# Kernel optimization log

Measured on AMD Instinct MI355X. Metric: run time of the kernel, lower is better.

Reference implementation:

```python
import jax, jax.numpy as jnp
import numpy as np

V, D, L, FF = 32000, 1024, 6, 4096
B, T = 2, 1024
EPS = 1e-6


def bitlinear(x, W):
    # W: [out, in]. Ternary quantize with straight-through estimator.
    s = jnp.maximum(jnp.mean(jnp.abs(W), axis=1, keepdims=True), 1e-5)
    w_q = jnp.clip(jnp.round(W / s), -1.0, 1.0)
    w = W + jax.lax.stop_gradient(w_q * s - W)
    return x @ w.T


def rmsnorm(x, g):
    return x * jax.lax.rsqrt(jnp.mean(x * x, axis=-1, keepdims=True) + EPS) * g


def time_mix(x, Wr, Wk, Wv, Wo, decay, lnx_w):
    # x: [B,T,D]
    r = jax.nn.sigmoid(bitlinear(x, Wr))
    k = bitlinear(x, Wk)
    v = bitlinear(x, Wv)
    dec = jax.nn.sigmoid(decay)                          # [D]
    log_decay = jnp.log(jnp.maximum(dec, 1e-7))          # [D]
    pos = jnp.arange(x.shape[1], dtype=x.dtype)          # [T]
    scale = jnp.exp(pos[:, None] * log_decay[None, :])   # [T,D]
    scaled = (k * v) / jnp.maximum(scale, 1e-10)[None]   # [B,T,D]
    state = jnp.cumsum(scaled, axis=1) * scale[None]     # [B,T,D]
    return bitlinear(rmsnorm(r * state, lnx_w), Wo)


def channel_mix(x, W1, W2, Wo):
    return bitlinear(jax.nn.silu(bitlinear(x, W1)) * bitlinear(x, W2), Wo)


def setup_inputs() -> dict:
    key = jax.random.key(0)
    ks = jax.random.split(key, 8)
    idx = jax.random.randint(ks[0], (B, T), 0, V)
    embed = jax.random.normal(ks[1], (V, D), jnp.float32) * 0.02

    def kaiming(k, shape):  # fan_out init: std = sqrt(2/out_features)
        return jax.random.normal(k, shape, jnp.float32) * np.sqrt(2.0 / shape[-2])

    kr, kk, kv, ko, k1, k2, koc = jax.random.split(ks[2], 7)
    return {
        "idx": idx,
        "embed": embed,
        "ln_in_w": jnp.ones((D,), jnp.float32),
        "ln1_w": jnp.ones((L, D), jnp.float32),
        "Wr": kaiming(kr, (L, D, D)),
        "Wk": kaiming(kk, (L, D, D)),
        "Wv": kaiming(kv, (L, D, D)),
        "Wo_t": kaiming(ko, (L, D, D)),
        "decay": jnp.full((L, D), 0.99, jnp.float32),
        "lnx_w": jnp.ones((L, D), jnp.float32),
        "ln2_w": jnp.ones((L, D), jnp.float32),
        "W1": kaiming(k1, (L, FF, D)),
        "W2": kaiming(k2, (L, FF, D)),
        "Wo_c": kaiming(koc, (L, D, FF)),
        "ln_out_w": jnp.ones((D,), jnp.float32),
    }


def reference(idx, embed, ln_in_w, ln1_w, Wr, Wk, Wv, Wo_t, decay, lnx_w,
              ln2_w, W1, W2, Wo_c, ln_out_w):
    h = rmsnorm(embed[idx], ln_in_w)  # [B,T,D]
    for i in range(L):
        h = h + time_mix(rmsnorm(h, ln1_w[i]), Wr[i], Wk[i], Wv[i], Wo_t[i],
                         decay[i], lnx_w[i])
        h = h + channel_mix(rmsnorm(h, ln2_w[i]), W1[i], W2[i], Wo_c[i])
    # weight-tied head
    return rmsnorm(h, ln_out_w) @ embed.T  # [B,T,V]
```

## Files before the change

kernel.cpp:

```cpp
#include <hip/hip_runtime.h>

typedef _Float16 f16;
typedef _Float16 f16x8 __attribute__((ext_vector_type(8)));
typedef _Float16 f16x4 __attribute__((ext_vector_type(4)));
typedef float f32x4 __attribute__((ext_vector_type(4)));
typedef int i32x4 __attribute__((ext_vector_type(4)));

static constexpr int BB = 2, T = 1024, D = 1024, FFD = 4096, V = 32000, NL = 6;
static constexpr int M = BB * T;
static constexpr int ROWS_PER_LAYER = 4*D + 2*FFD + D;
static constexpr size_t QL = 4ull*D*D + 2ull*FFD*D + (size_t)D*FFD;
static constexpr int NT = 64, CT = T / NT;
static constexpr int RKV = 3*D;

__device__ __forceinline__ void gload16(const f16* g, f16* l) {
  __builtin_amdgcn_global_load_lds(
      (const __attribute__((address_space(1))) void*)g,
      (__attribute__((address_space(3))) void*)l, 16, 0, 0);
}
__device__ __forceinline__ void gload16b(const void* g, void* l) {
  __builtin_amdgcn_global_load_lds(
      (const __attribute__((address_space(1))) void*)g,
      (__attribute__((address_space(3))) void*)l, 16, 0, 0);
}
template<int N> __device__ __forceinline__ void vm_wait() {
  static_assert(N >= 2 && N <= 4, "unsupported vmcnt");
  if constexpr (N == 2) asm volatile("s_waitcnt vmcnt(2)" ::: "memory");
  else if constexpr (N == 3) asm volatile("s_waitcnt vmcnt(3)" ::: "memory");
  else                       asm volatile("s_waitcnt vmcnt(4)" ::: "memory");
}
__device__ __forceinline__ void ring_barrier() {
  __builtin_amdgcn_s_barrier();
  __builtin_amdgcn_sched_barrier(0);
}

__global__ __launch_bounds__(256) void quant_kernel(
    const float* __restrict__ Wr, const float* __restrict__ Wk,
    const float* __restrict__ Wv, const float* __restrict__ Wo,
    const float* __restrict__ W1, const float* __restrict__ W2,
    const float* __restrict__ Woc, char* __restrict__ qw, float* __restrict__ scales)
{
  const int r = blockIdx.x, l = blockIdx.y;
  const float* base; int len; size_t dst;
  if (r < 4*D) {
    const int m = r >> 10, row = r & (D-1);
    const float* Wm = (m==0) ? Wr : (m==1) ? Wk : (m==2) ? Wv : Wo;
    base = Wm + (size_t)l*D*D + (size_t)row*D; len = D;
    dst = (size_t)l*QL + (size_t)m*D*D + (size_t)row*D;
  } else if (r < 4*D + 2*FFD) {
    int row = r - 4*D;
    const int m = row >= FFD; if (m) row -= FFD;
    const float* Wm = m ? W2 : W1;
    base = Wm + (size_t)l*FFD*D + (size_t)row*D; len = D;
    dst = (size_t)l*QL + 4ull*D*D + (size_t)m*FFD*D + (size_t)row*D;
  } else {
    const int row = r - (4*D + 2*FFD);
    base = Woc + (size_t)l*D*FFD + (size_t)row*FFD; len = FFD;
    dst = (size_t)l*QL + 4ull*D*D + 2ull*FFD*D + (size_t)row*FFD;
  }
  const int nv = len >> 10;
  float4 rv[4];
  float sum = 0.f;
  #pragma unroll 4
  for (int i = 0; i < 4; ++i) {
    if (i < nv) {
      rv[i] = reinterpret_cast<const float4*>(base)[threadIdx.x + i*256];
      sum += fabsf(rv[i].x) + fabsf(rv[i].y) + fabsf(rv[i].z) + fabsf(rv[i].w);
    }
  }
  #pragma unroll
  for (int off = 32; off > 0; off >>= 1) sum += __shfl_down(sum, off);
  __shared__ float red[4]; __shared__ float sbc;
  if ((threadIdx.x & 63) == 0) red[threadIdx.x >> 6] = sum;
  __syncthreads();
  if (threadIdx.x == 0) {
    const float s = fmaxf((red[0]+red[1]+red[2]+red[3]) / (float)len, 1e-5f);
    sbc = s;
    scales[(size_t)l*ROWS_PER_LAYER + r] = s;
  }
  __syncthreads();
  const float hs = 0.5f * sbc;
  #pragma unroll 4
  for (int i = 0; i < 4; ++i) {
    if (i < nv) {
      const float4 v = rv[i];
      char4 q;
      q.x = v.x > hs ? 1 : (v.x < -hs ? -1 : 0);
      q.y = v.y > hs ? 1 : (v.y < -hs ? -1 : 0);
      q.z = v.z > hs ? 1 : (v.z < -hs ? -1 : 0);
      q.w = v.w > hs ? 1 : (v.w < -hs ? -1 : 0);
      reinterpret_cast<char4*>(qw + dst)[threadIdx.x + i*256] = q;
    }
  }
}

__global__ __launch_bounds__(256) void quant_embed_kernel(
    const float* __restrict__ embed, char* __restrict__ q, float* __restrict__ sw)
{
  const int row = blockIdx.x;
  const float4 v = reinterpret_cast<const float4*>(embed + (size_t)row*D)[threadIdx.x];
  float mx = fmaxf(fmaxf(fabsf(v.x), fabsf(v.y)), fmaxf(fabsf(v.z), fabsf(v.w)));
  #pragma unroll
  for (int off = 32; off > 0; off >>= 1) mx = fmaxf(mx, __shfl_down(mx, off));
  __shared__ float red[4]; __shared__ float sbc;
  if ((threadIdx.x & 63) == 0) red[threadIdx.x >> 6] = mx;
  __syncthreads();
  if (threadIdx.x == 0) {
    const float m = fmaxf(fmaxf(red[0], red[1]), fmaxf(red[2], red[3]));
    const float s = fmaxf(m, 1e-8f) * (1.f/127.f);
    sbc = 1.f / s;
    sw[row] = s;
  }
  __syncthreads();
  const float inv = sbc;
  char4 o;
  o.x = (char)__float2int_rn(v.x * inv); o.y = (char)__float2int_rn(v.y * inv);
  o.z = (char)__float2int_rn(v.z * inv); o.w = (char)__float2int_rn(v.w * inv);
  reinterpret_cast<char4*>(q + (size_t)row*D)[threadIdx.x] = o;
}

__global__ __launch_bounds__(256) void embed_rms_kernel(
    const int* __restrict__ idx, const float* __restrict__ embed,
    const float* __restrict__ g, float* __restrict__ h)
{
  const int row = blockIdx.x;
  const int tok = idx[row];
  const float4 xv = reinterpret_cast<const float4*>(embed + (size_t)tok*D)[threadIdx.x];
  float ss = xv.x*xv.x + xv.y*xv.y + xv.z*xv.z + xv.w*xv.w;
  #pragma unroll
  for (int off = 32; off > 0; off >>= 1) ss += __shfl_down(ss, off);
  __shared__ float red[4];
  if ((threadIdx.x & 63) == 0) red[threadIdx.x >> 6] = ss;
  __syncthreads();
  const float mean = (red[0]+red[1]+red[2]+red[3]) * (1.f/(float)D);
  const float rn = rsqrtf(mean + 1e-6f);
  const float4 gv = reinterpret_cast<const float4*>(g)[threadIdx.x];
  float4 ov;
  ov.x = xv.x*rn*gv.x; ov.y = xv.y*rn*gv.y; ov.z = xv.z*rn*gv.z; ov.w = xv.w*rn*gv.w;
  reinterpret_cast<float4*>(h + (size_t)row*D)[threadIdx.x] = ov;
}

__global__ __launch_bounds__(256) void rms_i8_kernel(
    const float* __restrict__ x, const float* __restrict__ g,
    char* __restrict__ q, float* __restrict__ sx)
{
  const int row = blockIdx.x;
  const float4 xv = reinterpret_cast<const float4*>(x + (size_t)row*D)[threadIdx.x];
  const float4 gv = reinterpret_cast<const float4*>(g)[threadIdx.x];
  float4 pv;
  pv.x = xv.x*gv.x; pv.y = xv.y*gv.y; pv.z = xv.z*gv.z; pv.w = xv.w*gv.w;
  float ss = xv.x*xv.x + xv.y*xv.y + xv.z*xv.z + xv.w*xv.w;
  float mg = fmaxf(fmaxf(fabsf(pv.x), fabsf(pv.y)), fmaxf(fabsf(pv.z), fabsf(pv.w)));
  #pragma unroll
  for (int off = 32; off > 0; off >>= 1) {
    ss += __shfl_down(ss, off);
    mg = fmaxf(mg, __shfl_down(mg, off));
  }
  __shared__ float reds[4], redm[4]; __shared__ float sbc;
  if ((threadIdx.x & 63) == 0) { reds[threadIdx.x >> 6] = ss; redm[threadIdx.x >> 6] = mg; }
  __syncthreads();
  if (threadIdx.x == 0) {
    const float mean = (reds[0]+reds[1]+reds[2]+reds[3]) * (1.f/(float)D);
    const float rn = rsqrtf(mean + 1e-6f);
    const float vmax = rn * fmaxf(fmaxf(redm[0], redm[1]), fmaxf(redm[2], redm[3]));
    const float s = fmaxf(vmax, 1e-8f) * (1.f/127.f);
    sx[row] = s;
    sbc = rn / s;
  }
  __syncthreads();
  const float f = sbc;
  char4 o;
  o.x = (char)__float2int_rn(pv.x * f); o.y = (char)__float2int_rn(pv.y * f);
  o.z = (char)__float2int_rn(pv.z * f); o.w = (char)__float2int_rn(pv.w * f);
  reinterpret_cast<char4*>(q + (size_t)row*D)[threadIdx.x] = o;
}

__global__ __launch_bounds__(256) void rms_radd_i8_kernel(
    float* __restrict__ h, const float* __restrict__ p0,
    const float* __restrict__ p1, const float* __restrict__ g,
    char* __restrict__ q, float* __restrict__ sx)
{
  const int row = blockIdx.x;
  const size_t off = (size_t)row*D/4 + threadIdx.x;
  float4 hv = reinterpret_cast<const float4*>(h)[off];
  const float4 a = reinterpret_cast<const float4*>(p0)[off];
  const float4 b = reinterpret_cast<const float4*>(p1)[off];
  hv.x += a.x + b.x; hv.y += a.y + b.y; hv.z += a.z + b.z; hv.w += a.w + b.w;
  reinterpret_cast<float4*>(h)[off] = hv;
  const float4 gv = reinterpret_cast<const float4*>(g)[threadIdx.x];
  float4 pv;
  pv.x = hv.x*gv.x; pv.y = hv.y*gv.y; pv.z = hv.z*gv.z; pv.w = hv.w*gv.w;
  float ss = hv.x*hv.x + hv.y*hv.y + hv.z*hv.z + hv.w*hv.w;
  float mg = fmaxf(fmaxf(fabsf(pv.x), fabsf(pv.y)), fmaxf(fabsf(pv.z), fabsf(pv.w)));
  #pragma unroll
  for (int o2 = 32; o2 > 0; o2 >>= 1) {
    ss += __shfl_down(ss, o2);
    mg = fmaxf(mg, __shfl_down(mg, o2));
  }
  __shared__ float reds[4], redm[4]; __shared__ float sbc;
  if ((threadIdx.x & 63) == 0) { reds[threadIdx.x >> 6] = ss; redm[threadIdx.x >> 6] = mg; }
  __syncthreads();
  if (threadIdx.x == 0) {
    const float mean = (reds[0]+reds[1]+reds[2]+reds[3]) * (1.f/(float)D);
    const float rn = rsqrtf(mean + 1e-6f);
    const float vmax = rn * fmaxf(fmaxf(redm[0], redm[1]), fmaxf(redm[2], redm[3]));
    const float s = fmaxf(vmax, 1e-8f) * (1.f/127.f);
    sx[row] = s;
    sbc = rn / s;
  }
  __syncthreads();
  const float f = sbc;
  char4 o;
  o.x = (char)__float2int_rn(pv.x * f); o.y = (char)__float2int_rn(pv.y * f);
  o.z = (char)__float2int_rn(pv.z * f); o.w = (char)__float2int_rn(pv.w * f);
  reinterpret_cast<char4*>(q + (size_t)row*D)[threadIdx.x] = o;
}

__global__ __launch_bounds__(256) void quant_ffn_kernel(
    const f16* __restrict__ a, char* __restrict__ q, float* __restrict__ s)
{
  const int row = blockIdx.x;
  const size_t base = (size_t)row*(FFD/4);
  f16x4 v[4];
  float mx = 0.f;
  #pragma unroll
  for (int i = 0; i < 4; ++i) {
    v[i] = reinterpret_cast<const f16x4*>(a)[base + threadIdx.x + i*256];
    #pragma unroll
    for (int j = 0; j < 4; ++j) mx = fmaxf(mx, fabsf((float)v[i][j]));
  }
  #pragma unroll
  for (int off = 32; off > 0; off >>= 1) mx = fmaxf(mx, __shfl_down(mx, off));
  __shared__ float red[4]; __shared__ float sbc;
  if ((threadIdx.x & 63) == 0) red[threadIdx.x >> 6] = mx;
  __syncthreads();
  if (threadIdx.x == 0) {
    const float m = fmaxf(fmaxf(red[0], red[1]), fmaxf(red[2], red[3]));
    const float sr = fmaxf(m, 1e-8f) * (1.f/127.f);
    s[row] = sr;
    sbc = 1.f / sr;
  }
  __syncthreads();
  const float inv = sbc;
  #pragma unroll
  for (int i = 0; i < 4; ++i) {
    char4 o;
    o.x = (char)__float2int_rn((float)v[i][0] * inv);
    o.y = (char)__float2int_rn((float)v[i][1] * inv);
    o.z = (char)__float2int_rn((float)v[i][2] * inv);
    o.w = (char)__float2int_rn((float)v[i][3] * inv);
    reinterpret_cast<char4*>(q)[base + threadIdx.x + i*256] = o;
  }
}

__global__ __launch_bounds__(256) void scan1_kernel(
    const float* __restrict__ k, const float* __restrict__ v, int ld,
    const float* __restrict__ decay, float* __restrict__ part)
{
  const int d = blockIdx.x*256 + threadIdx.x;
  const int c = blockIdx.y, b = blockIdx.z;
  const float dec = 1.f / (1.f + expf(-decay[d]));
  const float ldc = logf(fmaxf(dec, 1e-7f));
  float sum = 0.f;
  const int row0 = b*T + c*CT;
  #pragma unroll 4
  for (int t = 0; t < CT; ++t) {
    const size_t i = (size_t)(row0 + t)*ld + d;
    const float scale = expf((float)(c*CT + t) * ldc);
    sum += (k[i] * v[i]) / fmaxf(scale, 1e-10f);
  }
  part[((size_t)b*NT + c)*D + d] = sum;
}

__global__ __launch_bounds__(256) void scan23_kernel(
    const float* __restrict__ r, const float* __restrict__ k,
    const float* __restrict__ v, int ld, const float* __restrict__ decay,
    const float* __restrict__ part, float* __restrict__ rs)
{
  const int d = blockIdx.x*256 + threadIdx.x;
  const int c = blockIdx.y, b = blockIdx.z;
  const float dec = 1.f / (1.f + expf(-decay[d]));
  const float ldc = logf(fmaxf(dec, 1e-7f));
  float cum = 0.f;
  for (int j = 0; j < c; ++j) cum += part[((size_t)b*NT + j)*D + d];
  const int row0 = b*T + c*CT;
  #pragma unroll 4
  for (int t = 0; t < CT; ++t) {
    const size_t i = (size_t)(row0 + t)*ld + d;
    const float scale = expf((float)(c*CT + t) * ldc);
    cum += (k[i] * v[i]) / fmaxf(scale, 1e-10f);
    rs[(size_t)(row0 + t)*D + d] = r[i] * (cum * scale);
  }
}

__global__ __launch_bounds__(256) void rms_f16_kernel(
    const float* __restrict__ x, const float* __restrict__ g, f16* __restrict__ o)
{
  const int row = blockIdx.x;
  const float4 xv = reinterpret_cast<const float4*>(x + (size_t)row*D)[threadIdx.x];
  float ss = xv.x*xv.x + xv.y*xv.y + xv.z*xv.z + xv.w*xv.w;
  #pragma unroll
  for (int off = 32; off > 0; off >>= 1) ss += __shfl_down(ss, off);
  __shared__ float red[4];
  if ((threadIdx.x & 63) == 0) red[threadIdx.x >> 6] = ss;
  __syncthreads();
  const float mean = (red[0]+red[1]+red[2]+red[3]) * (1.f/(float)D);
  const float rn = rsqrtf(mean + 1e-6f);
  const float4 gv = reinterpret_cast<const float4*>(g)[threadIdx.x];
  f16x4 ov;
  ov[0] = (f16)(xv.x*rn*gv.x); ov[1] = (f16)(xv.y*rn*gv.y);
  ov[2] = (f16)(xv.z*rn*gv.z); ov[3] = (f16)(xv.w*rn*gv.w);
  reinterpret_cast<f16x4*>(o + (size_t)row*D)[threadIdx.x] = ov;
}

__global__ __launch_bounds__(256) void scan2_kernel(float* __restrict__ part)
{
  const int d = blockIdx.x*256 + threadIdx.x;
  const int b = blockIdx.y;
  float run = 0.f;
  #pragma unroll 8
  for (int c = 0; c < NT; ++c) {
    const size_t i = ((size_t)b*NT + c)*D + d;
    const float t = part[i];
    part[i] = run;
    run += t;
  }
}

__global__ __launch_bounds__(256) void scan3_kernel(
    const float* __restrict__ r, const float* __restrict__ k,
    const float* __restrict__ v, int ld, const float* __restrict__ decay,
    const float* __restrict__ part, float* __restrict__ rs)
{
  const int d = blockIdx.x*256 + threadIdx.x;
  const int c = blockIdx.y, b = blockIdx.z;
  const float dec = 1.f / (1.f + expf(-decay[d]));
  const float ldc = logf(fmaxf(dec, 1e-7f));
  float cum = part[((size_t)b*NT + c)*D + d];
  const int row0 = b*T + c*CT;
  #pragma unroll 4
  for (int t = 0; t < CT; ++t) {
    const size_t i = (size_t)(row0 + t)*ld + d;
    const float scale = expf((float)(c*CT + t) * ldc);
    cum += (k[i] * v[i]) / fmaxf(scale, 1e-10f);
    rs[(size_t)(row0 + t)*D + d] = r[i] * (cum * scale);
  }
}

__global__ __launch_bounds__(256) void silumul_kernel(
    const f16* __restrict__ a, const f16* __restrict__ b, f16* __restrict__ o, int n4)
{
  const int i = blockIdx.x*256 + threadIdx.x;
  if (i >= n4) return;
  const f16x4 av = reinterpret_cast<const f16x4*>(a)[i];
  const f16x4 bv = reinterpret_cast<const f16x4*>(b)[i];
  f16x4 ov;
  #pragma unroll
  for (int j = 0; j < 4; ++j) {
    const float x = (float)av[j];
    ov[j] = (f16)((x / (1.f + expf(-x))) * (float)bv[j]);
  }
  reinterpret_cast<f16x4*>(o)[i] = ov;
}

__device__ __forceinline__ int xcd_swizzle(int fid, int nwg) {
  const int q = nwg >> 3, r = nwg & 7, x = fid & 7, o = fid >> 3;
  return (x < r ? x*(q+1) : r*(q+1) + (x-r)*q) + o;
}

template<int BM, int NW, int EPI, bool SPLITK = false>
__global__ __launch_bounds__(NW*64) void gemm_i8_kernel(
    const char* __restrict__ A, const char* __restrict__ Bq,
    const float* __restrict__ sx, const float* __restrict__ scl,
    const float* __restrict__ resid, float* __restrict__ outp, int N, int K)
{
  constexpr int WN = 2;
  constexpr int WM = NW / WN;
  constexpr int MF = BM / (WM*16);
  constexpr int ACALLS = BM / (16*NW);
  constexpr int BCALLS = 128 / (16*NW);
  constexpr int VCNT = ACALLS + BCALLS;
  __shared__ __align__(16) char As[3][BM*64];
  __shared__ __align__(16) char Bs[3][128*64];

  const int tid = threadIdx.x;
  const int wave = tid >> 6, lane = tid & 63;
  const int gx = gridDim.x, nwg = gx * gridDim.y;
  const int wg = xcd_swizzle(blockIdx.x + blockIdx.y*gx, nwg);
  const int m0 = (wg % gx) * BM, n0 = (wg / gx) * 128;
  const int lr = lane & 15, kg = lane >> 4;
  const int wm0 = (wave / WN) * (MF*16), wn0 = (wave % WN) * 64;
  const int grow = lane >> 2;
  const int gcol = (lane & 3) * 16;
  const char* Ab = A  + (size_t)(m0 + grow)*K + gcol;
  const char* Bb = Bq + (size_t)(n0 + grow)*K + gcol;

  int kbeg = 0, kend = K;
  size_t obase = 0;
  if (SPLITK) {
    const int kc = K / gridDim.z;
    kbeg = blockIdx.z * kc; kend = kbeg + kc;
    obase = (size_t)blockIdx.z * M * (size_t)N;
  }
  const int NKT = (kend - kbeg) / 64;

  auto stage = [&](int buf, int k0) {
    #pragma unroll
    for (int c = 0; c < ACALLS; ++c) {
      const int rb = (c*NW + wave) * 16;
      gload16b(Ab + (size_t)rb*K + k0, &As[buf][rb*64]);
    }
    #pragma unroll
    for (int c = 0; c < BCALLS; ++c) {
      const int rb = (c*NW + wave) * 16;
      gload16b(Bb + (size_t)rb*K + k0, &Bs[buf][rb*64]);
    }
  };

  i32x4 acc[MF][4] = {};
  stage(0, kbeg);
  stage(1, kbeg + 64);

  int cur = 0;
  for (int t = 0; t < NKT; ++t) {
    vm_wait<VCNT>();
    ring_barrier();
    if (t + 2 < NKT) {
      int nb = cur + 2; if (nb >= 3) nb -= 3;
      stage(nb, kbeg + (t + 2) * 64);
    }
    i32x4 af[MF], bf[4];
    #pragma unroll
    for (int i = 0; i < MF; ++i)
      af[i] = *reinterpret_cast<const i32x4*>(&As[cur][(wm0 + i*16 + lr)*64 + kg*16]);
    #pragma unroll
    for (int j = 0; j < 4; ++j)
      bf[j] = *reinterpret_cast<const i32x4*>(&Bs[cur][(wn0 + j*16 + lr)*64 + kg*16]);
    #pragma unroll
    for (int i = 0; i < MF; ++i)
      #pragma unroll
      for (int j = 0; j < 4; ++j)
        acc[i][j] = __builtin_amdgcn_mfma_i32_16x16x64_i8(af[i], bf[j], acc[i][j], 0, 0, 0);
    ++cur; if (cur == 3) cur = 0;
  }

  #pragma unroll
  for (int j = 0; j < 4; ++j) {
    const int col = n0 + wn0 + j*16 + lr;
    const float sv = scl[col];
    #pragma unroll
    for (int i = 0; i < MF; ++i) {
      #pragma unroll
      for (int e = 0; e < 4; ++e) {
        const int row = m0 + wm0 + i*16 + kg*4 + e;
        float y = (float)acc[i][j][e] * sx[row] * sv;
        if (EPI == 3 && col < D) y = 1.f / (1.f + expf(-y));
        if (EPI == 2) y += resid[(size_t)row*N + col];
        outp[obase + (size_t)row*N + col] = y;
      }
    }
  }
}

__global__ __launch_bounds__(512) void gemm_head_i8_kernel(
    const char* __restrict__ A, const char* __restrict__ Bq,
    const float* __restrict__ sx, const float* __restrict__ sw,
    float* __restrict__ out, int N, int K)
{
  constexpr int BM = 128, BN = 256;
  __shared__ __align__(16) char As[3][BM*64];
  __shared__ __align__(16) char Bs[3][BN*64];
  const int tid = threadIdx.x;
  const int wave = tid >> 6, lane = tid & 63;
  const int gx = gridDim.x, nwg = gx * gridDim.y;
  const int wg = xcd_swizzle(blockIdx.x + blockIdx.y*gx, nwg);
  const int m0 = (wg % gx) * BM, n0 = (wg / gx) * BN;
  const int lr = lane & 15, kg = lane >> 4;
  const int wm0 = (wave >> 2) * 64, wn0 = (wave & 3) * 64;
  const int grow = lane >> 2;
  const int gcol = (lane & 3) * 16;
  const char* Ab = A  + (size_t)(m0 + grow)*K + gcol;
  const char* Bb = Bq + (size_t)(n0 + grow)*K + gcol;

  auto stage = [&](int buf, int k0) {
    gload16b(Ab + (size_t)(wave*16)*K + k0, &As[buf][(wave*16)*64]);
    gload16b(Bb + (size_t)(wave*16)*K + k0, &Bs[buf][(wave*16)*64]);
    gload16b(Bb + (size_t)((wave+8)*16)*K + k0, &Bs[buf][((wave+8)*16)*64]);
  };

  i32x4 acc[4][4] = {};
  stage(0, 0);
  stage(1, 64);

  const int NKT = K / 64;
  int cur = 0;
  for (int t = 0; t < NKT; ++t) {
    vm_wait<3>();
    ring_barrier();
    if (t + 2 < NKT) {
      int nb = cur + 2; if (nb >= 3) nb -= 3;
      stage(nb, (t + 2) * 64);
    }
    i32x4 af[4], bf[4];
    #pragma unroll
    for (int i = 0; i < 4; ++i)
      af[i] = *reinterpret_cast<const i32x4*>(&As[cur][(wm0 + i*16 + lr)*64 + kg*16]);
    #pragma unroll
    for (int j = 0; j < 4; ++j)
      bf[j] = *reinterpret_cast<const i32x4*>(&Bs[cur][(wn0 + j*16 + lr)*64 + kg*16]);
    #pragma unroll
    for (int i = 0; i < 4; ++i)
      #pragma unroll
      for (int j = 0; j < 4; ++j)
        acc[i][j] = __builtin_amdgcn_mfma_i32_16x16x64_i8(af[i], bf[j], acc[i][j], 0, 0, 0);
    ++cur; if (cur == 3) cur = 0;
  }
  #pragma unroll
  for (int j = 0; j < 4; ++j) {
    const int col = n0 + wn0 + j*16 + lr;
    const float scw = sw[col];
    #pragma unroll
    for (int i = 0; i < 4; ++i) {
      #pragma unroll
      for (int e = 0; e < 4; ++e) {
        const int row = m0 + wm0 + i*16 + kg*4 + e;
        out[(size_t)row*N + col] = (float)acc[i][j][e] * sx[row] * scw;
      }
    }
  }
}

__global__ __launch_bounds__(512) void gemm_ffn_i8_kernel(
    const char* __restrict__ A, const char* __restrict__ B1, const char* __restrict__ B2,
    const float* __restrict__ sx, const float* __restrict__ s1, const float* __restrict__ s2,
    f16* __restrict__ outg, int N, int K)
{
  constexpr int BM = 128, BN = 128;
  __shared__ __align__(16) char As [3][BM*64];
  __shared__ __align__(16) char B1s[3][BN*64];
  __shared__ __align__(16) char B2s[3][BN*64];
  const int tid = threadIdx.x;
  const int wave = tid >> 6, lane = tid & 63;
  const int gx = gridDim.x, nwg = gx * gridDim.y;
  const int wg = xcd_swizzle(blockIdx.x + blockIdx.y*gx, nwg);
  const int m0 = (wg % gx) * BM, n0 = (wg / gx) * BN;
  const int lr = lane & 15, kg = lane >> 4;
  const int wm0 = (wave >> 1) * 32, wn0 = (wave & 1) * 64;
  const int grow = lane >> 2;
  const int gcol = (lane & 3) * 16;
  const char* Ab  = A  + (size_t)(m0 + grow)*K + gcol;
  const char* B1b = B1 + (size_t)(n0 + grow)*K + gcol;
  const char* B2b = B2 + (size_t)(n0 + grow)*K + gcol;

  auto stage = [&](int buf, int k0) {
    const int rb = wave * 16;
    gload16b(Ab  + (size_t)rb*K + k0, &As [buf][rb*64]);
    gload16b(B1b + (size_t)rb*K + k0, &B1s[buf][rb*64]);
    gload16b(B2b + (size_t)rb*K + k0, &B2s[buf][rb*64]);
  };

  i32x4 aca[2][4] = {};
  i32x4 acb[2][4] = {};
  stage(0, 0);
  stage(1, 64);

  const int NKT = K / 64;
  int cur = 0;
  for (int t = 0; t < NKT; ++t) {
    vm_wait<3>();
    ring_barrier();
    if (t + 2 < NKT) {
      int nb = cur + 2; if (nb >= 3) nb -= 3;
      stage(nb, (t + 2) * 64);
    }
    i32x4 af[2], b1f[4], b2f[4];
    #pragma unroll
    for (int i = 0; i < 2; ++i)
      af[i] = *reinterpret_cast<const i32x4*>(&As[cur][(wm0 + i*16 + lr)*64 + kg*16]);
    #pragma unroll
    for (int j = 0; j < 4; ++j) {
      b1f[j] = *reinterpret_cast<const i32x4*>(&B1s[cur][(wn0 + j*16 + lr)*64 + kg*16]);
      b2f[j] = *reinterpret_cast<const i32x4*>(&B2s[cur][(wn0 + j*16 + lr)*64 + kg*16]);
    }
    #pragma unroll
    for (int i = 0; i < 2; ++i)
      #pragma unroll
      for (int j = 0; j < 4; ++j) {
        aca[i][j] = __builtin_amdgcn_mfma_i32_16x16x64_i8(af[i], b1f[j], aca[i][j], 0, 0, 0);
        acb[i][j] = __builtin_amdgcn_mfma_i32_16x16x64_i8(af[i], b2f[j], acb[i][j], 0, 0, 0);
      }
    ++cur; if (cur == 3) cur = 0;
  }
  #pragma unroll
  for (int j = 0; j < 4; ++j) {
    const int col = n0 + wn0 + j*16 + lr;
    const float sa = s1[col], sb = s2[col];
    #pragma unroll
    for (int i = 0; i < 2; ++i) {
      #pragma unroll
      for (int e = 0; e < 4; ++e) {
        const int row = m0 + wm0 + i*16 + kg*4 + e;
        const float srow = sx[row];
        const float a = (float)aca[i][j][e] * srow * sa;
        const float b = (float)acb[i][j][e] * srow * sb;
        outg[(size_t)row*N + col] = (f16)((a / (1.f + expf(-a))) * b);
      }
    }
  }
}

__global__ __launch_bounds__(64) void scales_kernel(
    const float* __restrict__ Wr, const float* __restrict__ Wk,
    const float* __restrict__ Wv, const float* __restrict__ Wo,
    const float* __restrict__ W1, const float* __restrict__ W2,
    const float* __restrict__ Woc, float* __restrict__ s)
{
  const int r = blockIdx.x, l = blockIdx.y;
  const float* base; int len;
  if (r < 4*D) {
    const int m = r >> 10, row = r & (D-1);
    const float* Wm = (m==0) ? Wr : (m==1) ? Wk : (m==2) ? Wv : Wo;
    base = Wm + (size_t)l*D*D + (size_t)row*D; len = D;
  } else if (r < 4*D + 2*FFD) {
    int row = r - 4*D;
    const float* Wm = (row < FFD) ? W1 : W2;
    if (row >= FFD) row -= FFD;
    base = Wm + (size_t)l*FFD*D + (size_t)row*D; len = D;
  } else {
    const int row = r - (4*D + 2*FFD);
    base = Woc + (size_t)l*D*FFD + (size_t)row*FFD; len = FFD;
  }
  float sum = 0.f;
  for (int i = threadIdx.x; i < len; i += 64) sum += fabsf(base[i]);
  #pragma unroll
  for (int off = 32; off > 0; off >>= 1) sum += __shfl_down(sum, off);
  if (threadIdx.x == 0)
    s[(size_t)l*ROWS_PER_LAYER + r] = fmaxf(sum / (float)len, 1e-5f);
}

template<int BM, int EPI, bool QUANT, bool OUTF16>
__global__ __launch_bounds__(256) void gemm_bt_kernel(
    const f16* __restrict__ A, const float* __restrict__ Bw,
    const float* __restrict__ scl, const float* __restrict__ resid,
    void* __restrict__ outp, int N, int K)
{
  constexpr int BN = 128, LDT = 40;
  constexpr int MF = (BM == 128) ? 4 : 2;
  __shared__ f16 As[BM*LDT];
  __shared__ f16 Bs[BN*LDT];
  const int tid = threadIdx.x;
  const int m0 = blockIdx.y * BM, n0 = blockIdx.x * BN;
  const int wave = tid >> 6, lane = tid & 63;
  const int lr = lane & 15, kg = lane >> 4;
  const int wm0 = (wave >> 1) * (MF*16), wn0 = (wave & 1) * 64;
  f32x4 acc[MF][4] = {};
  for (int k0 = 0; k0 < K; k0 += 32) {
    #pragma unroll
    for (int c = 0; c < (BM*4)/256; ++c) {
      const int chunk = tid + c*256;
      const int row = chunk >> 2, c8 = (chunk & 3) << 3;
      *reinterpret_cast<f16x8*>(&As[row*LDT + c8]) =
        *reinterpret_cast<const f16x8*>(A + (size_t)(m0+row)*K + k0 + c8);
    }
    #pragma unroll
    for (int c = 0; c < 2; ++c) {
      const int chunk = tid + c*256;
      const int row = chunk >> 2, c8 = (chunk & 3) << 3;
      const float* bp = Bw + (size_t)(n0+row)*K + k0 + c8;
      const float4 f0 = *reinterpret_cast<const float4*>(bp);
      const float4 f1 = *reinterpret_cast<const float4*>(bp + 4);
      const float wv[8] = {f0.x,f0.y,f0.z,f0.w,f1.x,f1.y,f1.z,f1.w};
      f16x8 qv;
      if (QUANT) {
        const float hs = 0.5f * scl[n0+row];
        #pragma unroll
        for (int j = 0; j < 8; ++j)
          qv[j] = wv[j] > hs ? (f16)1.f : (wv[j] < -hs ? (f16)(-1.f) : (f16)0.f);
      } else {
        #pragma unroll
        for (int j = 0; j < 8; ++j) qv[j] = (f16)wv[j];
      }
      *reinterpret_cast<f16x8*>(&Bs[row*LDT + c8]) = qv;
    }
    __syncthreads();
    f16x8 af[MF], bf[4];
    #pragma unroll
    for (int i = 0; i < MF; ++i)
      af[i] = *reinterpret_cast<const f16x8*>(&As[(wm0 + i*16 + lr)*LDT + kg*8]);
    #pragma unroll
    for (int j = 0; j < 4; ++j)
      bf[j] = *reinterpret_cast<const f16x8*>(&Bs[(wn0 + j*16 + lr)*LDT + kg*8]);
    #pragma unroll
    for (int i = 0; i < MF; ++i)
      #pragma unroll
      for (int j = 0; j < 4; ++j)
        acc[i][j] = __builtin_amdgcn_mfma_f32_16x16x32_f16(af[i], bf[j], acc[i][j], 0, 0, 0);
    __syncthreads();
  }
  #pragma unroll
  for (int j = 0; j < 4; ++j) {
    const int col = n0 + wn0 + j*16 + lr;
    const float sv = QUANT ? scl[col] : 1.f;
    #pragma unroll
    for (int i = 0; i < MF; ++i) {
      #pragma unroll
      for (int e = 0; e < 4; ++e) {
        const int row = m0 + wm0 + i*16 + kg*4 + e;
        float y = acc[i][j][e] * sv;
        if (EPI == 1) y = 1.f / (1.f + expf(-y));
        if (EPI == 2) y += resid[(size_t)row*N + col];
        if (OUTF16) reinterpret_cast<f16*>(outp)[(size_t)row*N + col] = (f16)y;
        else        reinterpret_cast<float*>(outp)[(size_t)row*N + col] = y;
      }
    }
  }
}

extern "C" void kernel_launch(void* const* d_in, const int* in_sizes, int n_in,
                              void* d_out, int out_size, void* d_ws, size_t ws_size,
                              hipStream_t stream)
{
  (void)in_sizes; (void)n_in; (void)out_size;
  const int*   idx      = (const int*)  d_in[0];
  const float* embed    = (const float*)d_in[1];
  const float* ln_in_w  = (const float*)d_in[2];
  const float* ln1_w    = (const float*)d_in[3];
  const float* Wr       = (const float*)d_in[4];
  const float* Wk       = (const float*)d_in[5];
  const float* Wv       = (const float*)d_in[6];
  const float* Wo_t     = (const float*)d_in[7];
  const float* decay    = (const float*)d_in[8];
  const float* lnx_w    = (const float*)d_in[9];
  const float* ln2_w    = (const float*)d_in[10];
  const float* W1       = (const float*)d_in[11];
  const float* W2       = (const float*)d_in[12];
  const float* Wo_c     = (const float*)d_in[13];
  const float* ln_out_w = (const float*)d_in[14];
  float* out = (float*)d_out;

  char* p = (char*)d_ws;
  auto alloc = [&](size_t bytes) { void* q = (void*)p; p += (bytes + 255) & ~(size_t)255; return q; };
  float* h      = (float*)alloc((size_t)M*D*sizeof(float));
  f16*   xn     = (f16*)  alloc((size_t)M*D*sizeof(f16));
  float* rkv    = (float*)alloc((size_t)M*RKV*sizeof(float));
  float* rsb    = (float*)alloc((size_t)M*D*sizeof(float));
  f16*   abf    = (f16*)  alloc((size_t)M*FFD*sizeof(f16));
  f16*   bbf    = (f16*)  alloc((size_t)M*FFD*sizeof(f16));
  float* scales = (float*)alloc((size_t)NL*ROWS_PER_LAYER*sizeof(float));
  float* part   = (float*)alloc((size_t)BB*NT*D*sizeof(float));
  const size_t base_need = (size_t)(p - (char*)d_ws);
  const size_t fast_need = base_need + (NL*QL + 256)
      + ((size_t)V*D + 256) + (V*sizeof(float) + 256)
      + ((size_t)M*D + 256) + (M*sizeof(float) + 256)
      + ((size_t)M*FFD + 256) + (M*sizeof(float) + 256);

  embed_rms_kernel<<<M, 256, 0, stream>>>(idx, embed, ln_in_w, h);

  const dim3 gS(D/256, NT, BB);
  const dim3 gS2(D/256, BB);

  if (ws_size >= fast_need) {
    char*  qw8  = (char*) alloc(NL*QL);
    char*  emb8 = (char*) alloc((size_t)V*D);
    float* sw   = (float*)alloc((size_t)V*sizeof(float));
    char*  xn8  = (char*) alloc((size_t)M*D);
    float* sx   = (float*)alloc((size_t)M*sizeof(float));
    char*  abf8 = (char*) alloc((size_t)M*FFD);
    float* sax  = (float*)alloc((size_t)M*sizeof(float));
    quant_kernel<<<dim3(ROWS_PER_LAYER, NL), 256, 0, stream>>>(Wr, Wk, Wv, Wo_t, W1, W2, Wo_c, qw8, scales);
    quant_embed_kernel<<<V, 256, 0, stream>>>(embed, emb8, sw);

    const dim3 gRKV(M/128, RKV/128);
    const dim3 gO(M/64, D/128);
    const dim3 gOC(M/64, D/128, 2);
    const dim3 gFFN(M/128, FFD/128);
    const dim3 gHEAD(M/128, V/256);

    rms_i8_kernel<<<M, 256, 0, stream>>>(h, ln1_w, xn8, sx);
    for (int l = 0; l < NL; ++l) {
      const float* sl = scales + (size_t)l*ROWS_PER_LAYER;
      const char* qb = qw8 + (size_t)l*QL;
      const char *qrkv = qb, *qo = qb + 3ull*D*D;
      const char *q1 = qb + 4ull*D*D, *q2 = qb + 4ull*D*D + (size_t)FFD*D;
      const char *qoc = qb + 4ull*D*D + 2ull*(size_t)FFD*D;
      const float* dcy = decay + (size_t)l*D;
      gemm_i8_kernel<128,8,3><<<gRKV, 512, 0, stream>>>(xn8, qrkv, sx, sl, nullptr, rkv, RKV, D);
      scan1_kernel<<<gS, 256, 0, stream>>>(rkv + D, rkv + 2*D, RKV, dcy, part);
      scan23_kernel<<<gS, 256, 0, stream>>>(rkv, rkv + D, rkv + 2*D, RKV, dcy, part, rsb);
      rms_i8_kernel<<<M, 256, 0, stream>>>(rsb, lnx_w + (size_t)l*D, xn8, sx);
      gemm_i8_kernel<64,4,2><<<gO, 256, 0, stream>>>(xn8, qo, sx, sl + 3*D, h, h, D, D);
      rms_i8_kernel<<<M, 256, 0, stream>>>(h, ln2_w + (size_t)l*D, xn8, sx);
      gemm_ffn_i8_kernel<<<gFFN, 512, 0, stream>>>(xn8, q1, q2, sx, sl + 4*D, sl + 4*D + FFD, abf, FFD, D);
      quant_ffn_kernel<<<M, 256, 0, stream>>>(abf, abf8, sax);
      gemm_i8_kernel<64,4,0,true><<<gOC, 256, 0, stream>>>(abf8, qoc, sax, sl + 4*D + 2*FFD, nullptr, rkv, D, FFD);
      const float* gnext = (l + 1 < NL) ? (ln1_w + (size_t)(l+1)*D) : ln_out_w;
      rms_radd_i8_kernel<<<M, 256, 0, stream>>>(h, rkv, rkv + (size_t)M*D, gnext, xn8, sx);
    }
    gemm_head_i8_kernel<<<gHEAD, 512, 0, stream>>>(xn8, emb8, sx, sw, out, V, D);
  } else {
    float* rbuf = rkv;
    float* kbuf = rkv + (size_t)M*D;
    float* vbuf = rkv + 2ull*M*D;
    scales_kernel<<<dim3(ROWS_PER_LAYER, NL), 64, 0, stream>>>(Wr, Wk, Wv, Wo_t, W1, W2, Wo_c, scales);
    const dim3 gD(D/128, M/64);
    const dim3 gF(FFD/128, M/128);
    for (int l = 0; l < NL; ++l) {
      const float* sl = scales + (size_t)l*ROWS_PER_LAYER;
      const float* dcy = decay + (size_t)l*D;
      rms_f16_kernel<<<M, 256, 0, stream>>>(h, ln1_w + (size_t)l*D, xn);
      gemm_bt_kernel<64,1,true,false><<<gD, 256, 0, stream>>>(xn, Wr + (size_t)l*D*D, sl,       nullptr, rbuf, D, D);
      gemm_bt_kernel<64,0,true,false><<<gD, 256, 0, stream>>>(xn, Wk + (size_t)l*D*D, sl + D,   nullptr, kbuf, D, D);
      gemm_bt_kernel<64,0,true,false><<<gD, 256, 0, stream>>>(xn, Wv + (size_t)l*D*D, sl + 2*D, nullptr, vbuf, D, D);
      scan1_kernel<<<gS, 256, 0, stream>>>(kbuf, vbuf, D, dcy, part);
      scan2_kernel<<<gS2, 256, 0, stream>>>(part);
      scan3_kernel<<<gS, 256, 0, stream>>>(rbuf, kbuf, vbuf, D, dcy, part, rsb);
      rms_f16_kernel<<<M, 256, 0, stream>>>(rsb, lnx_w + (size_t)l*D, xn);
      gemm_bt_kernel<64,2,true,false><<<gD, 256, 0, stream>>>(xn, Wo_t + (size_t)l*D*D, sl + 3*D, h, h, D, D);
      rms_f16_kernel<<<M, 256, 0, stream>>>(h, ln2_w + (size_t)l*D, xn);
      gemm_bt_kernel<128,0,true,true><<<gF, 256, 0, stream>>>(xn, W1 + (size_t)l*FFD*D, sl + 4*D,       nullptr, abf, FFD, D);
      gemm_bt_kernel<128,0,true,true><<<gF, 256, 0, stream>>>(xn, W2 + (size_t)l*FFD*D, sl + 4*D + FFD, nullptr, bbf, FFD, D);
      silumul_kernel<<<(M*FFD/4)/256, 256, 0, stream>>>(abf, bbf, abf, M*FFD/4);
      gemm_bt_kernel<64,2,true,false><<<gD, 256, 0, stream>>>(abf, Wo_c + (size_t)l*D*FFD, sl + 4*D + 2*FFD, h, h, D, FFD);
    }
    rms_f16_kernel<<<M, 256, 0, stream>>>(h, ln_out_w, xn);
    gemm_bt_kernel<128,0,false,false><<<dim3(V/128, M/128), 256, 0, stream>>>(xn, embed, nullptr, nullptr, out, V, D);
  }
}
```

Before: 1.190 ms.

## Fuse FFN int8 quantization into gated GEMM epilogue with per-block scales

The gated FFN GEMM now quantizes its SiLU*gate output straight to int8, using a per-row scale for each 128-column block computed in the epilogue. This removes the f16 intermediate write/read and the separate quant_ffn kernel. A dedicated output-projection GEMM rescales its int32 accumulators into float every 128 K columns to apply those per-block scales. Separately, the head GEMM stages its output tile through LDS so it can write 16-byte coalesced stores. The trade-off is extra epilogue arithmetic and syncs, plus a finer-grained quantization scheme that changes numerics.

```diff
diff --git a/kernel.cpp b/kernel.cpp
--- a/kernel.cpp
+++ b/kernel.cpp
@@ -12,12 +12,8 @@
 static constexpr size_t QL = 4ull*D*D + 2ull*FFD*D + (size_t)D*FFD;
 static constexpr int NT = 64, CT = T / NT;
 static constexpr int RKV = 3*D;
-
-__device__ __forceinline__ void gload16(const f16* g, f16* l) {
-  __builtin_amdgcn_global_load_lds(
-      (const __attribute__((address_space(1))) void*)g,
-      (__attribute__((address_space(3))) void*)l, 16, 0, 0);
-}
+static constexpr int NKB = FFD / 128;
+
 __device__ __forceinline__ void gload16b(const void* g, void* l) {
   __builtin_amdgcn_global_load_lds(
       (const __attribute__((address_space(1))) void*)g,
@@ -216,43 +212,6 @@
   reinterpret_cast<char4*>(q + (size_t)row*D)[threadIdx.x] = o;
 }
 
-__global__ __launch_bounds__(256) void quant_ffn_kernel(
-    const f16* __restrict__ a, char* __restrict__ q, float* __restrict__ s)
-{
-  const int row = blockIdx.x;
-  const size_t base = (size_t)row*(FFD/4);
-  f16x4 v[4];
-  float mx = 0.f;
-  #pragma unroll
-  for (int i = 0; i < 4; ++i) {
-    v[i] = reinterpret_cast<const f16x4*>(a)[base + threadIdx.x + i*256];
-    #pragma unroll
-    for (int j = 0; j < 4; ++j) mx = fmaxf(mx, fabsf((float)v[i][j]));
-  }
-  #pragma unroll
-  for (int off = 32; off > 0; off >>= 1) mx = fmaxf(mx, __shfl_down(mx, off));
-  __shared__ float red[4]; __shared__ float sbc;
-  if ((threadIdx.x & 63) == 0) red[threadIdx.x >> 6] = mx;
-  __syncthreads();
-  if (threadIdx.x == 0) {
-    const float m = fmaxf(fmaxf(red[0], red[1]), fmaxf(red[2], red[3]));
-    const float sr = fmaxf(m, 1e-8f) * (1.f/127.f);
-    s[row] = sr;
-    sbc = 1.f / sr;
-  }
-  __syncthreads();
-  const float inv = sbc;
-  #pragma unroll
-  for (int i = 0; i < 4; ++i) {
-    char4 o;
-    o.x = (char)__float2int_rn((float)v[i][0] * inv);
-    o.y = (char)__float2int_rn((float)v[i][1] * inv);
-    o.z = (char)__float2int_rn((float)v[i][2] * inv);
-    o.w = (char)__float2int_rn((float)v[i][3] * inv);
-    reinterpret_cast<char4*>(q)[base + threadIdx.x + i*256] = o;
-  }
-}
-
 __global__ __launch_bounds__(256) void scan1_kernel(
     const float* __restrict__ k, const float* __restrict__ v, int ld,
     const float* __restrict__ decay, float* __restrict__ part)
@@ -368,7 +327,7 @@
   return (x < r ? x*(q+1) : r*(q+1) + (x-r)*q) + o;
 }
 
-template<int BM, int NW, int EPI, bool SPLITK = false>
+template<int BM, int NW, int EPI>
 __global__ __launch_bounds__(NW*64) void gemm_i8_kernel(
     const char* __restrict__ A, const char* __restrict__ Bq,
     const float* __restrict__ sx, const float* __restrict__ scl,
@@ -395,14 +354,7 @@
   const char* Ab = A  + (size_t)(m0 + grow)*K + gcol;
   const char* Bb = Bq + (size_t)(n0 + grow)*K + gcol;
 
-  int kbeg = 0, kend = K;
-  size_t obase = 0;
-  if (SPLITK) {
-    const int kc = K / gridDim.z;
-    kbeg = blockIdx.z * kc; kend = kbeg + kc;
-    obase = (size_t)blockIdx.z * M * (size_t)N;
-  }
-  const int NKT = (kend - kbeg) / 64;
+  const int NKT = K / 64;
 
   auto stage = [&](int buf, int k0) {
     #pragma unroll
@@ -418,6 +370,93 @@
   };
 
   i32x4 acc[MF][4] = {};
+  stage(0, 0);
+  stage(1, 64);
+
+  int cur = 0;
+  for (int t = 0; t < NKT; ++t) {
+    vm_wait<VCNT>();
+    ring_barrier();
+    if (t + 2 < NKT) {
+      int nb = cur + 2; if (nb >= 3) nb -= 3;
+      stage(nb, (t + 2) * 64);
+    }
+    i32x4 af[MF], bf[4];
+    #pragma unroll
+    for (int i = 0; i < MF; ++i)
+      af[i] = *reinterpret_cast<const i32x4*>(&As[cur][(wm0 + i*16 + lr)*64 + kg*16]);
+    #pragma unroll
+    for (int j = 0; j < 4; ++j)
+      bf[j] = *reinterpret_cast<const i32x4*>(&Bs[cur][(wn0 + j*16 + lr)*64 + kg*16]);
+    #pragma unroll
+    for (int i = 0; i < MF; ++i)
+      #pragma unroll
+      for (int j = 0; j < 4; ++j)
+        acc[i][j] = __builtin_amdgcn_mfma_i32_16x16x64_i8(af[i], bf[j], acc[i][j], 0, 0, 0);
+    ++cur; if (cur == 3) cur = 0;
+  }
+
+  #pragma unroll
+  for (int j = 0; j < 4; ++j) {
+    const int col = n0 + wn0 + j*16 + lr;
+    const float sv = scl[col];
+    #pragma unroll
+    for (int i = 0; i < MF; ++i) {
+      #pragma unroll
+      for (int e = 0; e < 4; ++e) {
+        const int row = m0 + wm0 + i*16 + kg*4 + e;
+        float y = (float)acc[i][j][e] * sx[row] * sv;
+        if (EPI == 3 && col < D) y = 1.f / (1.f + expf(-y));
+        if (EPI == 2) y += resid[(size_t)row*N + col];
+        outp[(size_t)row*N + col] = y;
+      }
+    }
+  }
+}
+
+__global__ __launch_bounds__(256) void gemm_oc_i8_kernel(
+    const char* __restrict__ A, const char* __restrict__ Bq,
+    const float* __restrict__ sax, const float* __restrict__ scl,
+    float* __restrict__ outp, int N, int K)
+{
+  constexpr int BM = 64, NW = 4, WN = 2;
+  constexpr int MF = 2;
+  constexpr int ACALLS = 1, BCALLS = 2, VCNT = 3;
+  __shared__ __align__(16) char As[3][BM*64];
+  __shared__ __align__(16) char Bs[3][128*64];
+
+  const int tid = threadIdx.x;
+  const int wave = tid >> 6, lane = tid & 63;
+  const int gx = gridDim.x, nwg = gx * gridDim.y;
+  const int wg = xcd_swizzle(blockIdx.x + blockIdx.y*gx, nwg);
+  const int m0 = (wg % gx) * BM, n0 = (wg / gx) * 128;
+  const int lr = lane & 15, kg = lane >> 4;
+  const int wm0 = (wave / WN) * (MF*16), wn0 = (wave % WN) * 64;
+  const int grow = lane >> 2;
+  const int gcol = (lane & 3) * 16;
+  const char* Ab = A  + (size_t)(m0 + grow)*K + gcol;
+  const char* Bb = Bq + (size_t)(n0 + grow)*K + gcol;
+
+  const int kc = K / gridDim.z;
+  const int kbeg = blockIdx.z * kc;
+  const size_t obase = (size_t)blockIdx.z * M * (size_t)N;
+  const int NKT = kc / 64;
+
+  auto stage = [&](int buf, int k0) {
+    #pragma unroll
+    for (int c = 0; c < ACALLS; ++c) {
+      const int rb = (c*NW + wave) * 16;
+      gload16b(Ab + (size_t)rb*K + k0, &As[buf][rb*64]);
+    }
+    #pragma unroll
+    for (int c = 0; c < BCALLS; ++c) {
+      const int rb = (c*NW + wave) * 16;
+      gload16b(Bb + (size_t)rb*K + k0, &Bs[buf][rb*64]);
+    }
+  };
+
+  i32x4 iacc[MF][4] = {};
+  f32x4 facc[MF][4] = {};
   stage(0, kbeg);
   stage(1, kbeg + 64);
 
@@ -440,7 +479,23 @@
     for (int i = 0; i < MF; ++i)
       #pragma unroll
       for (int j = 0; j < 4; ++j)
-        acc[i][j] = __builtin_amdgcn_mfma_i32_16x16x64_i8(af[i], bf[j], acc[i][j], 0, 0, 0);
+        iacc[i][j] = __builtin_amdgcn_mfma_i32_16x16x64_i8(af[i], bf[j], iacc[i][j], 0, 0, 0);
+    if (t & 1) {
+      const int kb = (kbeg >> 7) + (t >> 1);
+      #pragma unroll
+      for (int i = 0; i < MF; ++i) {
+        #pragma unroll
+        for (int e = 0; e < 4; ++e) {
+          const int row = m0 + wm0 + i*16 + kg*4 + e;
+          const float s = sax[(size_t)row*NKB + kb];
+          #pragma unroll
+          for (int j = 0; j < 4; ++j) {
+            facc[i][j][e] += (float)iacc[i][j][e] * s;
+            iacc[i][j][e] = 0;
+          }
+        }
+      }
+    }
     ++cur; if (cur == 3) cur = 0;
   }
 
@@ -453,10 +508,7 @@
       #pragma unroll
       for (int e = 0; e < 4; ++e) {
         const int row = m0 + wm0 + i*16 + kg*4 + e;
-        float y = (float)acc[i][j][e] * sx[row] * sv;
-        if (EPI == 3 && col < D) y = 1.f / (1.f + expf(-y));
-        if (EPI == 2) y += resid[(size_t)row*N + col];
-        outp[obase + (size_t)row*N + col] = y;
+        outp[obase + (size_t)row*N + col] = facc[i][j][e] * sv;
       }
     }
   }
@@ -468,8 +520,9 @@
     float* __restrict__ out, int N, int K)
 {
   constexpr int BM = 128, BN = 256;
-  __shared__ __align__(16) char As[3][BM*64];
-  __shared__ __align__(16) char Bs[3][BN*64];
+  __shared__ __align__(16) char smem[3*BM*64 + 3*BN*64];
+  char* AsB = smem;
+  char* BsB = smem + 3*BM*64;
   const int tid = threadIdx.x;
   const int wave = tid >> 6, lane = tid & 63;
   const int gx = gridDim.x, nwg = gx * gridDim.y;
@@ -483,9 +536,9 @@
   const char* Bb = Bq + (size_t)(n0 + grow)*K + gcol;
 
   auto stage = [&](int buf, int k0) {
-    gload16b(Ab + (size_t)(wave*16)*K + k0, &As[buf][(wave*16)*64]);
-    gload16b(Bb + (size_t)(wave*16)*K + k0, &Bs[buf][(wave*16)*64]);
-    gload16b(Bb + (size_t)((wave+8)*16)*K + k0, &Bs[buf][((wave+8)*16)*64]);
+    gload16b(Ab + (size_t)(wave*16)*K + k0, AsB + buf*BM*64 + (wave*16)*64);
+    gload16b(Bb + (size_t)(wave*16)*K + k0, BsB + buf*BN*64 + (wave*16)*64);
+    gload16b(Bb + (size_t)((wave+8)*16)*K + k0, BsB + buf*BN*64 + ((wave+8)*16)*64);
   };
 
   i32x4 acc[4][4] = {};
@@ -504,10 +557,10 @@
     i32x4 af[4], bf[4];
     #pragma unroll
     for (int i = 0; i < 4; ++i)
-      af[i] = *reinterpret_cast<const i32x4*>(&As[cur][(wm0 + i*16 + lr)*64 + kg*16]);
+      af[i] = *reinterpret_cast<const i32x4*>(AsB + cur*BM*64 + (wm0 + i*16 + lr)*64 + kg*16);
     #pragma unroll
     for (int j = 0; j < 4; ++j)
-      bf[j] = *reinterpret_cast<const i32x4*>(&Bs[cur][(wn0 + j*16 + lr)*64 + kg*16]);
+      bf[j] = *reinterpret_cast<const i32x4*>(BsB + cur*BN*64 + (wn0 + j*16 + lr)*64 + kg*16);
     #pragma unroll
     for (int i = 0; i < 4; ++i)
       #pragma unroll
@@ -515,17 +568,34 @@
         acc[i][j] = __builtin_amdgcn_mfma_i32_16x16x64_i8(af[i], bf[j], acc[i][j], 0, 0, 0);
     ++cur; if (cur == 3) cur = 0;
   }
-  #pragma unroll
-  for (int j = 0; j < 4; ++j) {
-    const int col = n0 + wn0 + j*16 + lr;
-    const float scw = sw[col];
-    #pragma unroll
-    for (int i = 0; i < 4; ++i) {
-      #pragma unroll
-      for (int e = 0; e < 4; ++e) {
-        const int row = m0 + wm0 + i*16 + kg*4 + e;
-        out[(size_t)row*N + col] = (float)acc[i][j][e] * sx[row] * scw;
+
+  float* otile = reinterpret_cast<float*>(smem);
+  #pragma unroll
+  for (int pass = 0; pass < 4; ++pass) {
+    __syncthreads();
+    if ((wave & 3) == pass) {
+      #pragma unroll
+      for (int j = 0; j < 4; ++j) {
+        const int col = n0 + wn0 + j*16 + lr;
+        const float scw = sw[col];
+        #pragma unroll
+        for (int i = 0; i < 4; ++i) {
+          #pragma unroll
+          for (int e = 0; e < 4; ++e) {
+            const int rb = wm0 + i*16 + kg*4 + e;
+            otile[rb*64 + j*16 + lr] = (float)acc[i][j][e] * sx[m0 + rb] * scw;
+          }
+        }
       }
+    }
+    __syncthreads();
+    const int slot0 = tid * 4;
+    #pragma unroll
+    for (int s = 0; s < 4; ++s) {
+      const int slot = slot0 + s;
+      const int r = slot >> 4, c4 = slot & 15;
+      *reinterpret_cast<f32x4*>(&out[(size_t)(m0 + r)*N + n0 + pass*64 + c4*4]) =
+          *reinterpret_cast<const f32x4*>(&otile[r*64 + c4*4]);
     }
   }
 }
@@ -533,12 +603,13 @@
 __global__ __launch_bounds__(512) void gemm_ffn_i8_kernel(
     const char* __restrict__ A, const char* __restrict__ B1, const char* __restrict__ B2,
     const float* __restrict__ sx, const float* __restrict__ s1, const float* __restrict__ s2,
-    f16* __restrict__ outg, int N, int K)
+    char* __restrict__ outg8, float* __restrict__ sax, int N, int K)
 {
   constexpr int BM = 128, BN = 128;
   __shared__ __align__(16) char As [3][BM*64];
   __shared__ __align__(16) char B1s[3][BN*64];
   __shared__ __align__(16) char B2s[3][BN*64];
+  __shared__ float rmx[2][BM];
   const int tid = threadIdx.x;
   const int wave = tid >> 6, lane = tid & 63;
   const int gx = gridDim.x, nwg = gx * gridDim.y;
@@ -591,22 +662,62 @@
       }
     ++cur; if (cur == 3) cur = 0;
   }
-  #pragma unroll
-  for (int j = 0; j < 4; ++j) {
-    const int col = n0 + wn0 + j*16 + lr;
-    const float sa = s1[col], sb = s2[col];
-    #pragma unroll
-    for (int i = 0; i < 2; ++i) {
-      #pragma unroll
-      for (int e = 0; e < 4; ++e) {
-        const int row = m0 + wm0 + i*16 + kg*4 + e;
-        const float srow = sx[row];
-        const float a = (float)aca[i][j][e] * srow * sa;
-        const float b = (float)acb[i][j][e] * srow * sb;
-        outg[(size_t)row*N + col] = (f16)((a / (1.f + expf(-a))) * b);
+
+  float gv[2][4][4];
+  float vmax[2][4];
+  #pragma unroll
+  for (int i = 0; i < 2; ++i)
+    #pragma unroll
+    for (int e = 0; e < 4; ++e) {
+      const int row = m0 + wm0 + i*16 + kg*4 + e;
+      const float srow = sx[row];
+      float mx = 0.f;
+      #pragma unroll
+      for (int j = 0; j < 4; ++j) {
+        const int col = n0 + wn0 + j*16 + lr;
+        const float a = (float)aca[i][j][e] * srow * s1[col];
+        const float b = (float)acb[i][j][e] * srow * s2[col];
+        const float gval = (a / (1.f + expf(-a))) * b;
+        gv[i][j][e] = gval;
+        mx = fmaxf(mx, fabsf(gval));
       }
-    }
-  }
+      vmax[i][e] = mx;
+    }
+  #pragma unroll
+  for (int i = 0; i < 2; ++i)
+    #pragma unroll
+    for (int e = 0; e < 4; ++e) {
+      float mx = vmax[i][e];
+      #pragma unroll
+      for (int off = 1; off < 16; off <<= 1) mx = fmaxf(mx, __shfl_xor(mx, off));
+      vmax[i][e] = mx;
+    }
+  __syncthreads();
+  if (lr == 0) {
+    #pragma unroll
+    for (int i = 0; i < 2; ++i)
+      #pragma unroll
+      for (int e = 0; e < 4; ++e)
+        rmx[wave & 1][wm0 + i*16 + kg*4 + e] = vmax[i][e];
+  }
+  __syncthreads();
+  const int nblk = n0 >> 7;
+  #pragma unroll
+  for (int i = 0; i < 2; ++i)
+    #pragma unroll
+    for (int e = 0; e < 4; ++e) {
+      const int rb = wm0 + i*16 + kg*4 + e;
+      const float rm = fmaxf(rmx[0][rb], rmx[1][rb]);
+      const float s = fmaxf(rm, 1e-8f) * (1.f/127.f);
+      const float inv = 1.f / s;
+      if ((wave & 1) == 0 && lr == 0)
+        sax[(size_t)(m0 + rb)*NKB + nblk] = s;
+      #pragma unroll
+      for (int j = 0; j < 4; ++j) {
+        const int col = n0 + wn0 + j*16 + lr;
+        outg8[(size_t)(m0 + rb)*N + col] = (char)__float2int_rn(gv[i][j][e] * inv);
+      }
+    }
 }
 
 __global__ __launch_bounds__(64) void scales_kernel(
@@ -752,7 +863,7 @@
   const size_t fast_need = base_need + (NL*QL + 256)
       + ((size_t)V*D + 256) + (V*sizeof(float) + 256)
       + ((size_t)M*D + 256) + (M*sizeof(float) + 256)
-      + ((size_t)M*FFD + 256) + (M*sizeof(float) + 256);
+      + ((size_t)M*FFD + 256) + ((size_t)M*NKB*sizeof(float) + 256);
 
   embed_rms_kernel<<<M, 256, 0, stream>>>(idx, embed, ln_in_w, h);
 
@@ -766,7 +877,7 @@
     char*  xn8  = (char*) alloc((size_t)M*D);
     float* sx   = (float*)alloc((size_t)M*sizeof(float));
     char*  abf8 = (char*) alloc((size_t)M*FFD);
-    float* sax  = (float*)alloc((size_t)M*sizeof(float));
+    float* sax  = (float*)alloc((size_t)M*NKB*sizeof(float));
     quant_kernel<<<dim3(ROWS_PER_LAYER, NL), 256, 0, stream>>>(Wr, Wk, Wv, Wo_t, W1, W2, Wo_c, qw8, scales);
     quant_embed_kernel<<<V, 256, 0, stream>>>(embed, emb8, sw);
 
@@ -790,9 +901,8 @@
       rms_i8_kernel<<<M, 256, 0, stream>>>(rsb, lnx_w + (size_t)l*D, xn8, sx);
       gemm_i8_kernel<64,4,2><<<gO, 256, 0, stream>>>(xn8, qo, sx, sl + 3*D, h, h, D, D);
       rms_i8_kernel<<<M, 256, 0, stream>>>(h, ln2_w + (size_t)l*D, xn8, sx);
-      gemm_ffn_i8_kernel<<<gFFN, 512, 0, stream>>>(xn8, q1, q2, sx, sl + 4*D, sl + 4*D + FFD, abf, FFD, D);
-      quant_ffn_kernel<<<M, 256, 0, stream>>>(abf, abf8, sax);
-      gemm_i8_kernel<64,4,0,true><<<gOC, 256, 0, stream>>>(abf8, qoc, sax, sl + 4*D + 2*FFD, nullptr, rkv, D, FFD);
+      gemm_ffn_i8_kernel<<<gFFN, 512, 0, stream>>>(xn8, q1, q2, sx, sl + 4*D, sl + 4*D + FFD, abf8, sax, FFD, D);
+      gemm_oc_i8_kernel<<<gOC, 256, 0, stream>>>(abf8, qoc, sax, sl + 4*D + 2*FFD, rkv, D, FFD);
       const float* gnext = (l + 1 < NL) ? (ln1_w + (size_t)(l+1)*D) : ln_out_w;
       rms_radd_i8_kernel<<<M, 256, 0, stream>>>(h, rkv, rkv + (size_t)M*D, gnext, xn8, sx);
     }
```

Result: slower. 1.221 ms (+2.6%).
